# Kernel optimization log

Hardware: AMD Instinct MI355X
Metric: run time of the kernel (lower is better)

## Reference

```python
import jax, jax.numpy as jnp
import numpy as np

N = 8192
IN_F = 512
OUT_F = 512
ALPHA = 0.2  # leaky relu slope


def setup_inputs() -> dict:
    key = jax.random.key(0)
    k1, k2, k3, k4, k5 = jax.random.split(key, 5)
    inp = jax.random.normal(k1, (N, IN_F), dtype=jnp.float32)
    adj = jax.random.randint(k2, (N, N), 0, 2, dtype=jnp.int32)
    # linear1: [in, out] + bias
    W1 = jax.random.normal(k3, (IN_F, OUT_F), dtype=jnp.float32) * (1.0 / np.sqrt(IN_F))
    b1 = jnp.zeros((OUT_F,), dtype=jnp.float32)
    # linear2: maps 2*out -> 1; split into the two halves acting on h_i and h_j
    a = jax.random.normal(k4, (2 * OUT_F,), dtype=jnp.float32) * (1.0 / np.sqrt(2 * OUT_F))
    a1 = a[:OUT_F]
    a2 = a[OUT_F:]
    b2 = jnp.zeros((), dtype=jnp.float32)
    return {"inp": inp, "adj": adj, "W1": W1, "b1": b1, "a1": a1, "a2": a2, "b2": b2}


def reference(inp, adj, W1, b1, a1, a2, b2):
    h = inp @ W1 + b1  # [N, out]
    # linear2(cat(h_i, h_j)) == h_i@a1 + h_j@a2 + b2 -> avoids the N*N*2F tensor
    e = jax.nn.leaky_relu((h @ a1)[:, None] + (h @ a2)[None, :] + b2, ALPHA)  # [N, N]
    attention = jnp.where(adj > 0, e, jnp.float32(-1e12))
    attention = jax.nn.softmax(attention, axis=1)
    h_prime = attention @ h  # [N, out]
    return jax.nn.elu(h_prime)  # concat=True
```

## Files before the change

kernel.cpp:

```cpp
#include <hip/hip_runtime.h>
#include <hip/hip_bf16.h>
#include <stdint.h>

#define NR 8192
#define FD 512
#define BM 64
#define BKC 128

typedef __attribute__((ext_vector_type(8))) short s8v;
typedef __attribute__((ext_vector_type(4))) float f32x4;

static __device__ __forceinline__ short bf16_rtne(float x) {
    union { float f; uint32_t u; } v; v.f = x;
    uint32_t r = (v.u + 0x7FFFu + ((v.u >> 16) & 1u)) >> 16;
    return (short)r;
}
static __device__ __forceinline__ float bf16_to_f32(short s) {
    union { uint32_t u; float f; } v; v.u = ((uint32_t)(uint16_t)s) << 16;
    return v.f;
}

__global__ void k_convert(const float* __restrict__ in, short* __restrict__ out) {
    int i = blockIdx.x * blockDim.x + threadIdx.x;
    float4 v = ((const float4*)in)[i];
    short4 s;
    s.x = bf16_rtne(v.x); s.y = bf16_rtne(v.y);
    s.z = bf16_rtne(v.z); s.w = bf16_rtne(v.w);
    ((short4*)out)[i] = s;
}

__global__ void k_w1t(const float* __restrict__ W1, short* __restrict__ W1T) {
    int i = blockIdx.x * 256 + threadIdx.x;
    int k = i & 511, n = i >> 9;
    W1T[(size_t)n * 512 + k] = bf16_rtne(W1[(size_t)k * 512 + n]);
}

__launch_bounds__(256)
__global__ void k_gemm_h(const short* __restrict__ A,
                         const short* __restrict__ BT,
                         const float* __restrict__ b1,
                         short* __restrict__ H,
                         short* __restrict__ HT2)
{
    const int lane = threadIdx.x & 63;
    const int wn   = threadIdx.x >> 6;
    const int m    = lane & 15;
    const int q    = lane >> 4;
    const int r0   = blockIdx.x * 32;
    const int c0   = blockIdx.y * 128 + wn * 32;

    f32x4 acc[2][2] = {};
#pragma unroll 1
    for (int k0 = 0; k0 < 512; k0 += 32) {
        s8v a[2], b[2];
#pragma unroll
        for (int rt = 0; rt < 2; ++rt)
            a[rt] = *(const s8v*)(A + (size_t)(r0 + rt * 16 + m) * 512 + k0 + q * 8);
#pragma unroll
        for (int nt = 0; nt < 2; ++nt)
            b[nt] = *(const s8v*)(BT + (size_t)(c0 + nt * 16 + m) * 512 + k0 + q * 8);
#pragma unroll
        for (int rt = 0; rt < 2; ++rt)
#pragma unroll
            for (int nt = 0; nt < 2; ++nt)
                acc[rt][nt] = __builtin_amdgcn_mfma_f32_16x16x32_bf16(a[rt], b[nt], acc[rt][nt], 0, 0, 0);
    }
    float b1v[2];
#pragma unroll
    for (int nt = 0; nt < 2; ++nt) b1v[nt] = b1[c0 + nt * 16 + m];

#pragma unroll
    for (int rt = 0; rt < 2; ++rt)
#pragma unroll
        for (int nt = 0; nt < 2; ++nt) {
            int col = c0 + nt * 16 + m;
            short4 hp;
#pragma unroll
            for (int r = 0; r < 4; ++r) {
                int row = r0 + rt * 16 + q * 4 + r;
                short hv = bf16_rtne(acc[rt][nt][r] + b1v[nt]);
                H[(size_t)row * 512 + col] = hv;
                ((short*)&hp)[r] = hv;
            }
            *(short4*)(HT2 + (size_t)blockIdx.x * (512 * 32) + (size_t)col * 32 + rt * 16 + q * 4) = hp;
        }
}

__global__ void k_f1f2(const short* __restrict__ H, const float* __restrict__ a1,
                       const float* __restrict__ a2, const float* __restrict__ b2,
                       float* __restrict__ f1, float* __restrict__ f2s)
{
    const int lane = threadIdx.x & 63;
    const int row  = blockIdx.x * 4 + (threadIdx.x >> 6);
    s8v hv = *(const s8v*)(H + (size_t)row * 512 + lane * 8);
    float4 a1l = ((const float4*)(a1 + lane * 8))[0];
    float4 a1h = ((const float4*)(a1 + lane * 8))[1];
    float4 a2l = ((const float4*)(a2 + lane * 8))[0];
    float4 a2h = ((const float4*)(a2 + lane * 8))[1];
    float hf[8];
#pragma unroll
    for (int i = 0; i < 8; ++i) hf[i] = bf16_to_f32(hv[i]);
    float s1 = hf[0] * a1l.x + hf[1] * a1l.y + hf[2] * a1l.z + hf[3] * a1l.w
             + hf[4] * a1h.x + hf[5] * a1h.y + hf[6] * a1h.z + hf[7] * a1h.w;
    float s2 = hf[0] * a2l.x + hf[1] * a2l.y + hf[2] * a2l.z + hf[3] * a2l.w
             + hf[4] * a2h.x + hf[5] * a2h.y + hf[6] * a2h.z + hf[7] * a2h.w;
#pragma unroll
    for (int o = 32; o > 0; o >>= 1) {
        s1 += __shfl_xor(s1, o);
        s2 += __shfl_xor(s2, o);
    }
    if (lane == 0) {
        f1[row]  = s1;
        f2s[row] = s2 + b2[0];
    }
}

__launch_bounds__(512, 4)
__global__ void k_attn(const int* __restrict__ adj,
                       const short* __restrict__ HT2,
                       const float* __restrict__ f1,
                       const float* __restrict__ f2s,
                       float* __restrict__ nump,
                       float* __restrict__ denomp)
{
    __shared__ __align__(16) short wt[2][BM * BKC];

    const int t    = threadIdx.x;
    const int lane = t & 63;
    const int w    = t >> 6;
    const int m    = lane & 15;
    const int q    = lane >> 4;

    const int js   = blockIdx.x & 3;
    const int band = blockIdx.x >> 2;
    const int r0   = band * BM;
    const int jb0  = js * 2048;

    const int prow = t >> 3;
    const int jg   = t & 7;

    const float f1v = f1[r0 + prow];
    const int*   adjp = adj + (size_t)(r0 + prow) * NR + jb0 + jg * 16;
    const float* f2p  = f2s + jb0 + jg * 16;

    f32x4 acc[4][4] = {};
    float dsum = 0.f;

    int4   aj[4];
    float4 fv[4];
#pragma unroll
    for (int g = 0; g < 4; ++g) {
        aj[g] = ((const int4*)adjp)[g];
        fv[g] = ((const float4*)f2p)[g];
    }

#pragma unroll 1
    for (int ch = 0; ch < 2048 / BKC; ++ch) {
        const int p = ch & 1;
        float wgt[16];
#pragma unroll
        for (int jj = 0; jj < 16; ++jj) {
            int   a  = ((const int*)aj)[jj];
            float s  = f1v + ((const float*)fv)[jj];
            float l  = fmaxf(s, 0.2f * s);
            float e  = __expf(l);
            float wv = (a != 0) ? e : 0.f;
            dsum += wv;
            wgt[jj] = wv;
        }
        s8v wv0, wv1;
#pragma unroll
        for (int jj = 0; jj < 8; ++jj) {
            wv0[jj] = bf16_rtne(wgt[jj]);
            wv1[jj] = bf16_rtne(wgt[8 + jj]);
        }
        const int sw = prow & 15;
        *(s8v*)&wt[p][prow * BKC + (((2 * jg) ^ sw) << 3)]     = wv0;
        *(s8v*)&wt[p][prow * BKC + (((2 * jg + 1) ^ sw) << 3)] = wv1;

        __syncthreads();

        const int chn = (ch + 1) & (2048 / BKC - 1);
#pragma unroll
        for (int g = 0; g < 4; ++g) {
            aj[g] = ((const int4*)(adjp + chn * BKC))[g];
            fv[g] = ((const float4*)(f2p + chn * BKC))[g];
        }

#pragma unroll
        for (int kk = 0; kk < 4; ++kk) {
            const int jt = (jb0 + ch * BKC + kk * 32) >> 5;
            const short* hb = HT2 + (size_t)jt * 16384 + q * 8;
            s8v af[4];
#pragma unroll
            for (int i = 0; i < 4; ++i) {
                int row = i * 16 + m;
                af[i] = *(const s8v*)&wt[p][row * BKC + (((kk * 4 + q) ^ m) << 3)];
            }
#pragma unroll
            for (int nt = 0; nt < 4; ++nt) {
                s8v b = *(const s8v*)(hb + (size_t)(w * 64 + nt * 16 + m) * 32);
#pragma unroll
                for (int i = 0; i < 4; ++i)
                    acc[i][nt] = __builtin_amdgcn_mfma_f32_16x16x32_bf16(af[i], b, acc[i][nt], 0, 0, 0);
            }
        }
    }

    dsum += __shfl_xor(dsum, 1);
    dsum += __shfl_xor(dsum, 2);
    dsum += __shfl_xor(dsum, 4);
    if (jg == 0) denomp[(size_t)js * NR + r0 + prow] = dsum;

    float* np = nump + (size_t)js * NR * FD;
#pragma unroll
    for (int i = 0; i < 4; ++i)
#pragma unroll
        for (int nt = 0; nt < 4; ++nt)
#pragma unroll
            for (int r = 0; r < 4; ++r) {
                int row = r0 + i * 16 + q * 4 + r;
                int col = w * 64 + nt * 16 + m;
                np[(size_t)row * FD + col] = acc[i][nt][r];
            }
}

__global__ void k_combine(const float* __restrict__ nump,
                          const float* __restrict__ denomp,
                          float* __restrict__ out)
{
    size_t e = ((size_t)blockIdx.x * 256 + threadIdx.x) * 4;
    int row = (int)(e >> 9);
    float4 n0 = *(const float4*)(nump + e);
    float4 n1 = *(const float4*)(nump + (size_t)NR * FD + e);
    float4 n2 = *(const float4*)(nump + (size_t)2 * NR * FD + e);
    float4 n3 = *(const float4*)(nump + (size_t)3 * NR * FD + e);
    float d = denomp[row] + denomp[NR + row] + denomp[2 * NR + row] + denomp[3 * NR + row];
    float inv = 1.0f / d;
    float4 o;
    o.x = (n0.x + n1.x + n2.x + n3.x) * inv;
    o.y = (n0.y + n1.y + n2.y + n3.y) * inv;
    o.z = (n0.z + n1.z + n2.z + n3.z) * inv;
    o.w = (n0.w + n1.w + n2.w + n3.w) * inv;
    o.x = (o.x > 0.f) ? o.x : (__expf(o.x) - 1.f);
    o.y = (o.y > 0.f) ? o.y : (__expf(o.y) - 1.f);
    o.z = (o.z > 0.f) ? o.z : (__expf(o.z) - 1.f);
    o.w = (o.w > 0.f) ? o.w : (__expf(o.w) - 1.f);
    *(float4*)(out + e) = o;
}

extern "C" void kernel_launch(void* const* d_in, const int* in_sizes, int n_in,
                              void* d_out, int out_size, void* d_ws, size_t ws_size,
                              hipStream_t stream) {
    const float* inp = (const float*)d_in[0];
    const int*   adj = (const int*)d_in[1];
    const float* W1  = (const float*)d_in[2];
    const float* b1  = (const float*)d_in[3];
    const float* a1  = (const float*)d_in[4];
    const float* a2  = (const float*)d_in[5];
    const float* b2  = (const float*)d_in[6];
    float* out = (float*)d_out;

    short* inp_bf = (short*)d_ws;
    short* w1t    = inp_bf + (size_t)NR * FD;
    short* h      = w1t + (size_t)FD * FD;
    short* ht2    = h + (size_t)NR * FD;
    float* f1     = (float*)(ht2 + (size_t)FD * NR);
    float* f2s    = f1 + NR;
    float* nump   = f2s + NR;
    float* denomp = nump + (size_t)4 * NR * FD;

    k_convert<<<(NR * FD / 4) / 256, 256, 0, stream>>>(inp, inp_bf);
    k_w1t<<<(FD * FD) / 256, 256, 0, stream>>>(W1, w1t);
    dim3 g1(NR / 32, FD / 128);
    k_gemm_h<<<g1, 256, 0, stream>>>(inp_bf, w1t, b1, h, ht2);
    k_f1f2<<<NR / 4, 256, 0, stream>>>(h, a1, a2, b2, f1, f2s);
    k_attn<<<128 * 4, 512, 0, stream>>>(adj, ht2, f1, f2s, nump, denomp);
    k_combine<<<(NR * FD / 4) / 256, 256, 0, stream>>>(nump, denomp, out);
}
```

Before: 526.9 us.

## Prepack adjacency matrix into bitmask before attention kernel

Adds a prepass kernel that reads the int32 adjacency matrix and packs it into a 1-bit-per-edge mask. The attention kernel then loads one 16-bit word per thread per chunk instead of sixteen int32 values. This is meant to cut memory traffic and register pressure inside the MFMA loop. The cost is an extra kernel launch that still streams the full adjacency matrix once, with no chance to overlap that read with compute.

```diff
diff --git a/kernel.cpp b/kernel.cpp
--- a/kernel.cpp
+++ b/kernel.cpp
@@ -18,6 +18,21 @@
 static __device__ __forceinline__ float bf16_to_f32(short s) {
     union { uint32_t u; float f; } v; v.u = ((uint32_t)(uint16_t)s) << 16;
     return v.f;
+}
+
+__global__ void k_prepack(const int* __restrict__ adj, uint32_t* __restrict__ bm) {
+    int t = blockIdx.x * 256 + threadIdx.x;
+    const int4* p = (const int4*)(adj + (size_t)t * 32);
+    uint32_t word = 0;
+#pragma unroll
+    for (int g = 0; g < 8; ++g) {
+        int4 v = p[g];
+        word |= (uint32_t)(v.x != 0) << (g * 4);
+        word |= (uint32_t)(v.y != 0) << (g * 4 + 1);
+        word |= (uint32_t)(v.z != 0) << (g * 4 + 2);
+        word |= (uint32_t)(v.w != 0) << (g * 4 + 3);
+    }
+    bm[t] = word;
 }
 
 __global__ void k_convert(const float* __restrict__ in, short* __restrict__ out) {
@@ -116,7 +131,7 @@
 }
 
 __launch_bounds__(512, 4)
-__global__ void k_attn(const int* __restrict__ adj,
+__global__ void k_attn(const uint32_t* __restrict__ bm,
                        const short* __restrict__ HT2,
                        const float* __restrict__ f1,
                        const float* __restrict__ f2s,
@@ -140,19 +155,16 @@
     const int jg   = t & 7;
 
     const float f1v = f1[r0 + prow];
-    const int*   adjp = adj + (size_t)(r0 + prow) * NR + jb0 + jg * 16;
-    const float* f2p  = f2s + jb0 + jg * 16;
+    const uint16_t* bmp = (const uint16_t*)(bm + (size_t)(r0 + prow) * 256) + (jb0 >> 4) + jg;
+    const float*    f2p = f2s + jb0 + jg * 16;
 
     f32x4 acc[4][4] = {};
     float dsum = 0.f;
 
-    int4   aj[4];
+    uint32_t bits = bmp[0];
     float4 fv[4];
 #pragma unroll
-    for (int g = 0; g < 4; ++g) {
-        aj[g] = ((const int4*)adjp)[g];
-        fv[g] = ((const float4*)f2p)[g];
-    }
+    for (int g = 0; g < 4; ++g) fv[g] = ((const float4*)f2p)[g];
 
 #pragma unroll 1
     for (int ch = 0; ch < 2048 / BKC; ++ch) {
@@ -160,11 +172,10 @@
         float wgt[16];
 #pragma unroll
         for (int jj = 0; jj < 16; ++jj) {
-            int   a  = ((const int*)aj)[jj];
             float s  = f1v + ((const float*)fv)[jj];
             float l  = fmaxf(s, 0.2f * s);
             float e  = __expf(l);
-            float wv = (a != 0) ? e : 0.f;
+            float wv = ((bits >> jj) & 1u) ? e : 0.f;
             dsum += wv;
             wgt[jj] = wv;
         }
@@ -181,11 +192,9 @@
         __syncthreads();
 
         const int chn = (ch + 1) & (2048 / BKC - 1);
-#pragma unroll
-        for (int g = 0; g < 4; ++g) {
-            aj[g] = ((const int4*)(adjp + chn * BKC))[g];
-            fv[g] = ((const float4*)(f2p + chn * BKC))[g];
-        }
+        bits = bmp[chn * 8];
+#pragma unroll
+        for (int g = 0; g < 4; ++g) fv[g] = ((const float4*)(f2p + chn * BKC))[g];
 
 #pragma unroll
         for (int kk = 0; kk < 4; ++kk) {
@@ -261,20 +270,22 @@
     const float* b2  = (const float*)d_in[6];
     float* out = (float*)d_out;
 
-    short* inp_bf = (short*)d_ws;
-    short* w1t    = inp_bf + (size_t)NR * FD;
-    short* h      = w1t + (size_t)FD * FD;
-    short* ht2    = h + (size_t)NR * FD;
-    float* f1     = (float*)(ht2 + (size_t)FD * NR);
-    float* f2s    = f1 + NR;
-    float* nump   = f2s + NR;
-    float* denomp = nump + (size_t)4 * NR * FD;
-
+    short*    inp_bf = (short*)d_ws;
+    short*    w1t    = inp_bf + (size_t)NR * FD;
+    short*    h      = w1t + (size_t)FD * FD;
+    short*    ht2    = h + (size_t)NR * FD;
+    uint32_t* bmw    = (uint32_t*)(ht2 + (size_t)FD * NR);
+    float*    f1     = (float*)(bmw + (size_t)NR * 256);
+    float*    f2s    = f1 + NR;
+    float*    nump   = f2s + NR;
+    float*    denomp = nump + (size_t)4 * NR * FD;
+
+    k_prepack<<<NR * 256 / 256, 256, 0, stream>>>(adj, bmw);
     k_convert<<<(NR * FD / 4) / 256, 256, 0, stream>>>(inp, inp_bf);
     k_w1t<<<(FD * FD) / 256, 256, 0, stream>>>(W1, w1t);
     dim3 g1(NR / 32, FD / 128);
     k_gemm_h<<<g1, 256, 0, stream>>>(inp_bf, w1t, b1, h, ht2);
     k_f1f2<<<NR / 4, 256, 0, stream>>>(h, a1, a2, b2, f1, f2s);
-    k_attn<<<128 * 4, 512, 0, stream>>>(adj, ht2, f1, f2s, nump, denomp);
+    k_attn<<<128 * 4, 512, 0, stream>>>(bmw, ht2, f1, f2s, nump, denomp);
     k_combine<<<(NR * FD / 4) / 256, 256, 0, stream>>>(nump, denomp, out);
 }
```

Result: slower. 565.9 us (+7.4%).
